# Kernel tuning notes

Measured on AMD Instinct MI355X. Metric: run time of the kernel, lower is better.

Reference implementation:

```python
import jax, jax.numpy as jnp
import numpy as np

D_MODEL = 256
N_HEADS = 8
D_K = 16
LN_EPS = 1e-5


def setup_inputs() -> dict:
    key = jax.random.key(0)
    ks = jax.random.split(key, 10)
    B, S = 4, 2048
    inp = {
        "input_Q": jax.random.normal(ks[0], (B, S, D_MODEL), dtype=jnp.float32),
        "input_K": jax.random.normal(ks[1], (B, S, D_MODEL), dtype=jnp.float32),
        "input_V": jax.random.normal(ks[2], (B, S, D_MODEL), dtype=jnp.float32),
        "attn_mask": jax.random.randint(ks[3], (B, S, S), 0, 2) == 1,
        # learned params (torch Linear weight [out,in] stored here as [in,out])
        "Wq": jax.random.normal(ks[4], (D_MODEL, N_HEADS * D_K), dtype=jnp.float32) * (1.0 / np.sqrt(D_MODEL)),
        "Wk": jax.random.normal(ks[5], (D_MODEL, N_HEADS * D_K), dtype=jnp.float32) * (1.0 / np.sqrt(D_MODEL)),
        "Wv": jax.random.normal(ks[6], (D_MODEL, N_HEADS * D_K), dtype=jnp.float32) * (1.0 / np.sqrt(D_MODEL)),
        "Wfc": jax.random.normal(ks[7], (N_HEADS * D_K, D_MODEL), dtype=jnp.float32) * (1.0 / np.sqrt(N_HEADS * D_K)),
        "ln_gamma": jnp.ones((D_MODEL,), dtype=jnp.float32),
        "ln_beta": jnp.zeros((D_MODEL,), dtype=jnp.float32),
    }
    return inp


def reference(input_Q, input_K, input_V, attn_mask, Wq, Wk, Wv, Wfc, ln_gamma, ln_beta):
    B, S, _ = input_Q.shape
    # projections -> [B, H, S, d_k]
    Q = (input_Q @ Wq).reshape(B, S, N_HEADS, D_K).transpose(0, 2, 1, 3)
    K = (input_K @ Wk).reshape(B, S, N_HEADS, D_K).transpose(0, 2, 1, 3)
    V = (input_V @ Wv).reshape(B, S, N_HEADS, D_K).transpose(0, 2, 1, 3)
    # scores [B, H, S, S], masked softmax
    scores = jnp.einsum("bhqd,bhkd->bhqk", Q, K) / np.sqrt(D_K).astype(np.float32)
    scores = jnp.where(attn_mask[:, None, :, :], jnp.float32(-1e9), scores)
    attn = jax.nn.softmax(scores, axis=-1)
    context = jnp.einsum("bhqk,bhkd->bhqd", attn, V)
    context = context.transpose(0, 2, 1, 3).reshape(B, S, N_HEADS * D_K)
    out = context @ Wfc
    # LayerNorm (no residual in the original module)
    mu = jnp.mean(out, axis=-1, keepdims=True)
    var = jnp.var(out, axis=-1, keepdims=True)
    out = (out - mu) * jax.lax.rsqrt(var + LN_EPS) * ln_gamma + ln_beta
    return out
```

## Files before the change

### kernel.cpp

```cpp
#include <hip/hip_runtime.h>
#include <hip/hip_bf16.h>

#define S_LEN 2048
#define BATCH 4
#define NH 8
#define DK 16
#define DM 256
#define DP 128
#define L2E 1.4426950408889634f
#define MAGIC_BOOL 0x600DB001

typedef short bf16x8 __attribute__((ext_vector_type(8)));
typedef short short4v __attribute__((ext_vector_type(4)));
typedef float f32x16 __attribute__((ext_vector_type(16)));

__device__ __forceinline__ short f2bf(float x) {
    __hip_bfloat16 h = __float2bfloat16(x);
    return __builtin_bit_cast(short, h);
}

union Frag { bf16x8 v; short4v h2[2]; };

__global__ __launch_bounds__(256) void setup(
    const unsigned int* __restrict__ mrawu, int* __restrict__ flag,
    const float* __restrict__ Wq, const float* __restrict__ Wk,
    const float* __restrict__ Wv, short* __restrict__ Wt)
{
    const int bi = blockIdx.x;
    if (bi < 1024) {
        unsigned int u = mrawu[bi * 256 + threadIdx.x];
        if (u & 0xFFFFFF00u) *flag = MAGIC_BOOL;
    } else {
        const int tid = (bi - 1024) * 256 + threadIdx.x;
        const int m = tid >> 15;
        const int rem = tid & 32767;
        const int k = rem >> 7, c = rem & 127;
        const float* W = (m == 0) ? Wq : (m == 1) ? Wk : Wv;
        const float scale = (m == 0) ? 0.25f * L2E : 1.0f;
        Wt[((size_t)m * 128 + c) * 256 + k] = f2bf(W[(size_t)k * 128 + c] * scale);
    }
}

__global__ __launch_bounds__(256) void phase1(
    const void* __restrict__ mraw, const int* __restrict__ flag,
    unsigned long long* __restrict__ ms64,
    const float* __restrict__ Xq, const float* __restrict__ Xk, const float* __restrict__ Xv,
    const short* __restrict__ Wt,
    short* __restrict__ Qb, short* __restrict__ Kb, short* __restrict__ Vb)
{
    __shared__ short xs_s[32 * 260];
    const int bi = blockIdx.x;
    const int t = threadIdx.x;

    if (bi < 768) {
        const int inp = bi >> 8;
        const int s0 = (bi & 255) * 32;
        {
            const float* xsrc = ((inp == 0) ? Xq : (inp == 1) ? Xk : Xv)
                              + (size_t)(s0 + (t >> 3)) * 256 + (t & 7) * 32;
            short* xdst = &xs_s[(t >> 3) * 260 + (t & 7) * 32];
            #pragma unroll
            for (int u = 0; u < 8; ++u) {
                float4 xv = *(const float4*)(xsrc + u * 4);
                short4v o = { f2bf(xv.x), f2bf(xv.y), f2bf(xv.z), f2bf(xv.w) };
                *(short4v*)(xdst + u * 4) = o;
            }
        }
        __syncthreads();

        const int wave = t >> 6, lane = t & 63;
        const int lq = lane & 31, hi = lane >> 5;
        const int c = wave * 32 + lq;
        const short* wrow = Wt + ((size_t)inp * 128 + c) * 256;

        f32x16 acc;
        #pragma unroll
        for (int i = 0; i < 16; ++i) acc[i] = 0.f;

        #pragma unroll
        for (int kb = 0; kb < 16; ++kb) {
            Frag af, bf_;
            af.h2[0]  = *(const short4v*)&xs_s[lq * 260 + kb*16 + 4*hi];
            af.h2[1]  = *(const short4v*)&xs_s[lq * 260 + kb*16 + 8 + 4*hi];
            bf_.h2[0] = *(const short4v*)(wrow + kb*16 + 4*hi);
            bf_.h2[1] = *(const short4v*)(wrow + kb*16 + 8 + 4*hi);
            acc = __builtin_amdgcn_mfma_f32_32x32x16_bf16(af.v, bf_.v, acc, 0, 0, 0);
        }

        const int b = s0 >> 11, sl = s0 & (S_LEN - 1);
        const int h = c >> 4, d = c & 15;
        if (inp < 2) {
            short* dst = (inp == 0) ? Qb : Kb;
            #pragma unroll
            for (int r = 0; r < 16; ++r) {
                const int s = sl + (r & 3) + 8*(r >> 2) + 4*hi;
                dst[(((size_t)(b * NH + h)) * S_LEN + s) * DK + d] = f2bf(acc[r]);
            }
        } else {
            short* vb = Vb + (((size_t)(b * NH + h)) * 32 + d) * S_LEN + sl;
            #pragma unroll
            for (int g = 0; g < 4; ++g) {
                short4v vv = { f2bf(acc[4*g]), f2bf(acc[4*g+1]), f2bf(acc[4*g+2]), f2bf(acc[4*g+3]) };
                *(short4v*)(vb + 8*g + 4*hi) = vv;
            }
        }
    } else if (bi < 1280) {
        const int tid = (bi - 768) * 256 + t;
        const int bh = tid >> 12;
        const int rem = tid & 4095;
        const int row = 16 + (rem >> 11) * 4;
        const int s = rem & 2047;
        Vb[((size_t)bh * 32 + row) * S_LEN + s] = (short)0x3F80;
    } else {
        const int lane = t & 63;
        const size_t kbase = ((size_t)(bi - 1280) * 4 + (t >> 6)) * 256;
        const int isInt = (*flag != MAGIC_BOOL);

        int v[4];
        if (isInt) {
            const int* p = (const int*)mraw + kbase + lane;
            #pragma unroll
            for (int g = 0; g < 4; ++g) v[g] = p[g * 64];
        } else {
            const unsigned char* p = (const unsigned char*)mraw + kbase + lane;
            #pragma unroll
            for (int g = 0; g < 4; ++g) v[g] = p[g * 64];
        }

        const int src = 32*((lane>>5)&1) + 4*((lane>>4)&1) + 8*((lane>>2)&3) + (lane&3);
        const size_t row = kbase >> 11;
        const int koff0 = (int)(kbase & 2047);

        #pragma unroll
        for (int g = 0; g < 4; ++g) {
            const unsigned long long W = __ballot(v[g] != 0);
            const unsigned long long W2 = __ballot((int)((W >> src) & 1ull));
            if (lane == 0) {
                const int koff = koff0 + g * 64;
                ms64[(size_t)(koff >> 7) * (BATCH*S_LEN*2) + row*2 + ((koff >> 6) & 1)] = W2;
            }
        }
    }
}

__global__ __launch_bounds__(256, 8) void attn_mfma(
    const short* __restrict__ Qb, const short* __restrict__ Kb, const short* __restrict__ Vb,
    const unsigned int* __restrict__ ms, float* __restrict__ pacc, float* __restrict__ pl)
{
    __shared__ short kt_s[128 * 20];
    __shared__ short vt_s[32 * 132];

    const int bh = blockIdx.y;
    const int b = bh >> 3;
    const int z = blockIdx.z;
    const int t = threadIdx.x;
    const int wave = t >> 6, lane = t & 63;
    const int lq = lane & 31, hi = lane >> 5;
    const int qrow = blockIdx.x * 128 + wave * 32 + lq;
    const int hish = hi * 16;

    Frag qf;
    {
        const short* qp = Qb + ((size_t)bh * S_LEN + qrow) * DK;
        qf.h2[0] = *(const short4v*)(qp + 4*hi);
        qf.h2[1] = *(const short4v*)(qp + 8 + 4*hi);
    }

    f32x16 acc;
    #pragma unroll
    for (int i = 0; i < 16; ++i) acc[i] = 0.f;

    const short* kbase = Kb + (size_t)bh * S_LEN * DK;
    const short* vbase = Vb + (size_t)bh * 32 * S_LEN;
    const unsigned int* mbase = ms + ((size_t)b * S_LEN + qrow) * 4;

    const int tiles = (S_LEN / 128) / gridDim.z;
    const int t0 = z * tiles, t1 = t0 + tiles;

    for (int tile = t0; tile < t1; ++tile) {
        const int k0 = tile * 128;

        {
            const uint4 kv = *(const uint4*)(kbase + (size_t)k0 * DK + t * 8);
            short* kdst = &kt_s[(t >> 1) * 20 + (t & 1) * 8];
            *(uint2*)(kdst)     = *(uint2*)&kv;
            *(uint2*)(kdst + 4) = *((uint2*)&kv + 1);

            const short* vsrc = vbase + (size_t)(t >> 3) * S_LEN + k0 + (t & 7) * 16;
            uint4 v0 = *(const uint4*)(vsrc);
            uint4 v1 = *(const uint4*)(vsrc + 8);
            short* vdst = &vt_s[(t >> 3) * 132 + (t & 7) * 16];
            *(uint2*)(vdst)      = *(uint2*)&v0;
            *(uint2*)(vdst + 4)  = *((uint2*)&v0 + 1);
            *(uint2*)(vdst + 8)  = *(uint2*)&v1;
            *(uint2*)(vdst + 12) = *((uint2*)&v1 + 1);
        }
        __syncthreads();

        const uint4 mw = *(const uint4*)(mbase + (size_t)tile * (BATCH * S_LEN * 4));

        #pragma unroll
        for (int kt = 0; kt < 4; ++kt) {
            const unsigned int W = ((kt==0)?mw.x:(kt==1)?mw.y:(kt==2)?mw.z:mw.w) >> hish;
            f32x16 ci;
            #pragma unroll
            for (int r = 0; r < 16; ++r)
                ci[r] = __int_as_float(((int)(W << (31 - r)) >> 31) & 0xC2C80000);

            Frag kf;
            kf.h2[0] = *(const short4v*)&kt_s[(kt*32 + lq) * 20 + 4*hi];
            kf.h2[1] = *(const short4v*)&kt_s[(kt*32 + lq) * 20 + 8 + 4*hi];
            f32x16 p = __builtin_amdgcn_mfma_f32_32x32x16_bf16(kf.v, qf.v, ci, 0, 0, 0);

            #pragma unroll
            for (int r = 0; r < 16; ++r) p[r] = __builtin_amdgcn_exp2f(p[r]);

            #pragma unroll
            for (int j = 0; j < 2; ++j) {
                union { bf16x8 v; short s[8]; } pf;
                #pragma unroll
                for (int e = 0; e < 8; ++e) pf.s[e] = f2bf(p[j*8 + e]);
                Frag vf;
                const int vo = lq * 132 + (kt*2 + j) * 16 + 4*hi;
                vf.h2[0] = *(const short4v*)&vt_s[vo];
                vf.h2[1] = *(const short4v*)&vt_s[vo + 8];
                acc = __builtin_amdgcn_mfma_f32_32x32x16_bf16(vf.v, pf.v, acc, 0, 0, 0);
            }
        }
        __syncthreads();
    }

    float* pb = pacc + (((size_t)z * (BATCH*NH) + bh) * S_LEN + qrow) * 16;
    float4 o1 = { acc[0], acc[1], acc[2], acc[3] };
    float4 o2 = { acc[4], acc[5], acc[6], acc[7] };
    *(float4*)(pb + 4*hi) = o1;
    *(float4*)(pb + 8 + 4*hi) = o2;
    if (hi == 0) pl[((size_t)z * (BATCH*NH) + bh) * S_LEN + qrow] = acc[8];
}

__global__ __launch_bounds__(256) void fc_ln(
    const float* __restrict__ pacc, const float* __restrict__ pl, int ns,
    const float* __restrict__ Wfc,
    const float* __restrict__ gamma, const float* __restrict__ beta,
    float* __restrict__ out)
{
    __shared__ float cs[8][DP];
    __shared__ float ys[8][256];
    __shared__ float red[16];
    const int t = threadIdx.x;
    const int row0 = blockIdx.x * 8;

    {
        const int idx = t * 4;
        const int r = idx >> 7, k = idx & 127;
        const int grow = row0 + r;
        const int b = grow >> 11, q = grow & (S_LEN - 1);
        const int h = k >> 4, d0 = k & 15;
        float4 s = {0.f, 0.f, 0.f, 0.f};
        float L = 0.f;
        for (int z = 0; z < ns; ++z) {
            const size_t o = ((size_t)z * (BATCH*NH) + b * NH + h) * S_LEN + q;
            const float4 a = *(const float4*)(pacc + o * 16 + d0);
            s.x += a.x; s.y += a.y; s.z += a.z; s.w += a.w;
            L += pl[o];
        }
        const float inv = 1.0f / L;
        float4 o4 = { s.x * inv, s.y * inv, s.z * inv, s.w * inv };
        *(float4*)&cs[r][k] = o4;
    }
    __syncthreads();

    float acc[8] = {0,0,0,0,0,0,0,0};
    for (int k = 0; k < DP; k += 4) {
        const float w0 = Wfc[(k+0)*DM + t];
        const float w1 = Wfc[(k+1)*DM + t];
        const float w2 = Wfc[(k+2)*DM + t];
        const float w3 = Wfc[(k+3)*DM + t];
        #pragma unroll
        for (int r = 0; r < 8; ++r) {
            float4 x = *(const float4*)&cs[r][k];
            acc[r] = fmaf(x.x, w0, fmaf(x.y, w1, fmaf(x.z, w2, fmaf(x.w, w3, acc[r]))));
        }
    }

    #pragma unroll
    for (int r = 0; r < 8; ++r) ys[r][t] = acc[r];
    __syncthreads();

    const int w = t >> 6, lj = t & 63;
    #pragma unroll
    for (int rr = 0; rr < 2; ++rr) {
        const int r = w * 2 + rr;
        float a0 = ys[r][lj], a1 = ys[r][lj+64], a2 = ys[r][lj+128], a3 = ys[r][lj+192];
        float s1 = a0 + a1 + a2 + a3;
        float s2 = a0*a0 + a1*a1 + a2*a2 + a3*a3;
        #pragma unroll
        for (int off = 32; off; off >>= 1) {
            s1 += __shfl_xor(s1, off);
            s2 += __shfl_xor(s2, off);
        }
        if (lj == 0) {
            float mu = s1 * (1.0f/256.0f);
            float var = s2 * (1.0f/256.0f) - mu*mu;
            red[r*2]     = mu;
            red[r*2 + 1] = rsqrtf(var + 1e-5f);
        }
    }
    __syncthreads();

    const float g = gamma[t], be = beta[t];
    #pragma unroll
    for (int r = 0; r < 8; ++r) {
        float y = (acc[r] - red[r*2]) * red[r*2 + 1];
        out[(size_t)(row0 + r) * DM + t] = fmaf(y, g, be);
    }
}

extern "C" void kernel_launch(void* const* d_in, const int* in_sizes, int n_in,
                              void* d_out, int out_size, void* d_ws, size_t ws_size,
                              hipStream_t stream)
{
    const float* Xq = (const float*)d_in[0];
    const float* Xk = (const float*)d_in[1];
    const float* Xv = (const float*)d_in[2];
    const void* mask_raw = d_in[3];
    const float* Wq  = (const float*)d_in[4];
    const float* Wk  = (const float*)d_in[5];
    const float* Wv  = (const float*)d_in[6];
    const float* Wfc = (const float*)d_in[7];
    const float* gamma = (const float*)d_in[8];
    const float* beta  = (const float*)d_in[9];
    float* out = (float*)d_out;

    const size_t headsz = (size_t)BATCH * NH * S_LEN * DK;
    const size_t maskelems = (size_t)BATCH * S_LEN * S_LEN;

    char* wsb = (char*)d_ws;
    short* Qb = (short*)wsb;
    short* Kb = Qb + headsz;
    short* Vb = Kb + headsz;
    unsigned short* msk = (unsigned short*)(Vb + 2 * headsz);
    short* Wt = (short*)(msk + maskelems / 16);
    float* pacc = (float*)(Wt + 3 * 128 * 256);
    size_t ns = 4;
    {
        const size_t fixed = (size_t)((char*)pacc - wsb);
        while (ns > 1 && fixed + ns * ((size_t)BATCH*NH*S_LEN*17*4) + 64 > ws_size)
            ns >>= 1;
    }
    float* pl = pacc + ns * (size_t)BATCH * NH * S_LEN * 16;
    int* flag = (int*)(pl + ns * (size_t)BATCH * NH * S_LEN);

    setup<<<dim3(1408), dim3(256), 0, stream>>>(
        (const unsigned int*)mask_raw, flag, Wq, Wk, Wv, Wt);
    phase1<<<dim3(768 + 512 + (unsigned)(maskelems / 1024)), dim3(256), 0, stream>>>(
        mask_raw, flag, (unsigned long long*)msk, Xq, Xk, Xv, Wt, Qb, Kb, Vb);
    attn_mfma<<<dim3(S_LEN / 128, BATCH * NH, (unsigned)ns), dim3(256), 0, stream>>>(
        Qb, Kb, Vb, (const unsigned int*)msk, pacc, pl);
    fc_ln<<<dim3(BATCH * S_LEN / 8), dim3(256), 0, stream>>>(pacc, pl, (int)ns, Wfc, gamma, beta, out);
}
```

Measured before the change: 85.71 us.

## Store Q transposed, drop mask bit-permute ballot, coarsen mask packing blocks

Q is now written in a transposed [bh][d][s] layout using vectorized short4 stores like V, and the attention kernel gathers it with strided scalar loads. The mask packer drops its second permuting ballot and stores raw ballot words. The attention kernel instead decodes the bit order per row from two 64-bit words. Each mask-packing wave now handles 1024 elements instead of 256, so fewer blocks are launched. The X staging loads are also reordered to be fully coalesced. The goal is to cut scattered global stores and ballot work in phase1, at the cost of uncoalesced Q loads that happen once per thread.

New measurement: 81.65 us. 4.7% less time.

```diff
diff --git a/kernel.cpp b/kernel.cpp
--- a/kernel.cpp
+++ b/kernel.cpp
@@ -46,7 +46,7 @@
     unsigned long long* __restrict__ ms64,
     const float* __restrict__ Xq, const float* __restrict__ Xk, const float* __restrict__ Xv,
     const short* __restrict__ Wt,
-    short* __restrict__ Qb, short* __restrict__ Kb, short* __restrict__ Vb)
+    short* __restrict__ Qt, short* __restrict__ Kb, short* __restrict__ Vb)
 {
     __shared__ short xs_s[32 * 260];
     const int bi = blockIdx.x;
@@ -56,14 +56,14 @@
         const int inp = bi >> 8;
         const int s0 = (bi & 255) * 32;
         {
-            const float* xsrc = ((inp == 0) ? Xq : (inp == 1) ? Xk : Xv)
-                              + (size_t)(s0 + (t >> 3)) * 256 + (t & 7) * 32;
-            short* xdst = &xs_s[(t >> 3) * 260 + (t & 7) * 32];
+            const float* xbase = ((inp == 0) ? Xq : (inp == 1) ? Xk : Xv) + (size_t)s0 * 256;
             #pragma unroll
             for (int u = 0; u < 8; ++u) {
-                float4 xv = *(const float4*)(xsrc + u * 4);
+                const int idx = u * 1024 + t * 4;
+                const int row = idx >> 8, col = idx & 255;
+                float4 xv = *(const float4*)(xbase + idx);
                 short4v o = { f2bf(xv.x), f2bf(xv.y), f2bf(xv.z), f2bf(xv.w) };
-                *(short4v*)(xdst + u * 4) = o;
+                *(short4v*)&xs_s[row * 260 + col] = o;
             }
         }
         __syncthreads();
@@ -89,19 +89,20 @@
 
         const int b = s0 >> 11, sl = s0 & (S_LEN - 1);
         const int h = c >> 4, d = c & 15;
-        if (inp < 2) {
-            short* dst = (inp == 0) ? Qb : Kb;
+        if (inp == 1) {
             #pragma unroll
             for (int r = 0; r < 16; ++r) {
                 const int s = sl + (r & 3) + 8*(r >> 2) + 4*hi;
-                dst[(((size_t)(b * NH + h)) * S_LEN + s) * DK + d] = f2bf(acc[r]);
+                Kb[(((size_t)(b * NH + h)) * S_LEN + s) * DK + d] = f2bf(acc[r]);
             }
         } else {
-            short* vb = Vb + (((size_t)(b * NH + h)) * 32 + d) * S_LEN + sl;
+            short* base = (inp == 0)
+                ? Qt + (((size_t)(b * NH + h)) * 16 + d) * S_LEN + sl
+                : Vb + (((size_t)(b * NH + h)) * 32 + d) * S_LEN + sl;
             #pragma unroll
             for (int g = 0; g < 4; ++g) {
                 short4v vv = { f2bf(acc[4*g]), f2bf(acc[4*g+1]), f2bf(acc[4*g+2]), f2bf(acc[4*g+3]) };
-                *(short4v*)(vb + 8*g + 4*hi) = vv;
+                *(short4v*)(base + 8*g + 4*hi) = vv;
             }
         }
     } else if (bi < 1280) {
@@ -113,39 +114,37 @@
         Vb[((size_t)bh * 32 + row) * S_LEN + s] = (short)0x3F80;
     } else {
         const int lane = t & 63;
-        const size_t kbase = ((size_t)(bi - 1280) * 4 + (t >> 6)) * 256;
+        const size_t kbase = ((size_t)(bi - 1280) * 4 + (t >> 6)) * 1024;
         const int isInt = (*flag != MAGIC_BOOL);
 
-        int v[4];
+        int v[16];
         if (isInt) {
             const int* p = (const int*)mraw + kbase + lane;
             #pragma unroll
-            for (int g = 0; g < 4; ++g) v[g] = p[g * 64];
+            for (int g = 0; g < 16; ++g) v[g] = p[g * 64];
         } else {
             const unsigned char* p = (const unsigned char*)mraw + kbase + lane;
             #pragma unroll
-            for (int g = 0; g < 4; ++g) v[g] = p[g * 64];
-        }
-
-        const int src = 32*((lane>>5)&1) + 4*((lane>>4)&1) + 8*((lane>>2)&3) + (lane&3);
+            for (int g = 0; g < 16; ++g) v[g] = p[g * 64];
+        }
+
         const size_t row = kbase >> 11;
         const int koff0 = (int)(kbase & 2047);
 
         #pragma unroll
-        for (int g = 0; g < 4; ++g) {
+        for (int g = 0; g < 16; ++g) {
             const unsigned long long W = __ballot(v[g] != 0);
-            const unsigned long long W2 = __ballot((int)((W >> src) & 1ull));
             if (lane == 0) {
                 const int koff = koff0 + g * 64;
-                ms64[(size_t)(koff >> 7) * (BATCH*S_LEN*2) + row*2 + ((koff >> 6) & 1)] = W2;
+                ms64[(size_t)(koff >> 7) * (BATCH*S_LEN*2) + row*2 + ((koff >> 6) & 1)] = W;
             }
         }
     }
 }
 
 __global__ __launch_bounds__(256, 8) void attn_mfma(
-    const short* __restrict__ Qb, const short* __restrict__ Kb, const short* __restrict__ Vb,
-    const unsigned int* __restrict__ ms, float* __restrict__ pacc, float* __restrict__ pl)
+    const short* __restrict__ Qt, const short* __restrict__ Kb, const short* __restrict__ Vb,
+    const unsigned long long* __restrict__ ms64, float* __restrict__ pacc, float* __restrict__ pl)
 {
     __shared__ short kt_s[128 * 20];
     __shared__ short vt_s[32 * 132];
@@ -157,13 +156,15 @@
     const int wave = t >> 6, lane = t & 63;
     const int lq = lane & 31, hi = lane >> 5;
     const int qrow = blockIdx.x * 128 + wave * 32 + lq;
-    const int hish = hi * 16;
 
     Frag qf;
     {
-        const short* qp = Qb + ((size_t)bh * S_LEN + qrow) * DK;
-        qf.h2[0] = *(const short4v*)(qp + 4*hi);
-        qf.h2[1] = *(const short4v*)(qp + 8 + 4*hi);
+        const short* qt = Qt + (size_t)bh * 16 * S_LEN + qrow;
+        #pragma unroll
+        for (int j = 0; j < 4; ++j) {
+            qf.h2[0][j] = qt[(size_t)(4*hi + j) * S_LEN];
+            qf.h2[1][j] = qt[(size_t)(8 + 4*hi + j) * S_LEN];
+        }
     }
 
     f32x16 acc;
@@ -172,7 +173,7 @@
 
     const short* kbase = Kb + (size_t)bh * S_LEN * DK;
     const short* vbase = Vb + (size_t)bh * 32 * S_LEN;
-    const unsigned int* mbase = ms + ((size_t)b * S_LEN + qrow) * 4;
+    const unsigned long long* mbase = ms64 + ((size_t)b * S_LEN + qrow) * 2;
 
     const int tiles = (S_LEN / 128) / gridDim.z;
     const int t0 = z * tiles, t1 = t0 + tiles;
@@ -197,15 +198,19 @@
         }
         __syncthreads();
 
-        const uint4 mw = *(const uint4*)(mbase + (size_t)tile * (BATCH * S_LEN * 4));
+        const unsigned long long* mw = mbase + (size_t)tile * (BATCH * S_LEN * 2);
+        const unsigned long long W64a = mw[0], W64b = mw[1];
 
         #pragma unroll
         for (int kt = 0; kt < 4; ++kt) {
-            const unsigned int W = ((kt==0)?mw.x:(kt==1)?mw.y:(kt==2)?mw.z:mw.w) >> hish;
+            const unsigned int W = (unsigned int)(((kt < 2) ? W64a : W64b)
+                                                  >> (32*(kt & 1) + 4*hi));
             f32x16 ci;
             #pragma unroll
-            for (int r = 0; r < 16; ++r)
-                ci[r] = __int_as_float(((int)(W << (31 - r)) >> 31) & 0xC2C80000);
+            for (int r = 0; r < 16; ++r) {
+                const int bit = (r & 3) + 8*(r >> 2);
+                ci[r] = __int_as_float(((int)(W << (31 - bit)) >> 31) & 0xC2C80000);
+            }
 
             Frag kf;
             kf.h2[0] = *(const short4v*)&kt_s[(kt*32 + lq) * 20 + 4*hi];
@@ -336,11 +341,11 @@
     const size_t maskelems = (size_t)BATCH * S_LEN * S_LEN;
 
     char* wsb = (char*)d_ws;
-    short* Qb = (short*)wsb;
-    short* Kb = Qb + headsz;
+    short* Qt = (short*)wsb;
+    short* Kb = Qt + headsz;
     short* Vb = Kb + headsz;
-    unsigned short* msk = (unsigned short*)(Vb + 2 * headsz);
-    short* Wt = (short*)(msk + maskelems / 16);
+    unsigned long long* msk = (unsigned long long*)(Vb + 2 * headsz);
+    short* Wt = (short*)(msk + maskelems / 64);
     float* pacc = (float*)(Wt + 3 * 128 * 256);
     size_t ns = 4;
     {
@@ -353,9 +358,9 @@
 
     setup<<<dim3(1408), dim3(256), 0, stream>>>(
         (const unsigned int*)mask_raw, flag, Wq, Wk, Wv, Wt);
-    phase1<<<dim3(768 + 512 + (unsigned)(maskelems / 1024)), dim3(256), 0, stream>>>(
-        mask_raw, flag, (unsigned long long*)msk, Xq, Xk, Xv, Wt, Qb, Kb, Vb);
+    phase1<<<dim3(768 + 512 + (unsigned)(maskelems / 4096)), dim3(256), 0, stream>>>(
+        mask_raw, flag, msk, Xq, Xk, Xv, Wt, Qt, Kb, Vb);
     attn_mfma<<<dim3(S_LEN / 128, BATCH * NH, (unsigned)ns), dim3(256), 0, stream>>>(
-        Qb, Kb, Vb, (const unsigned int*)msk, pacc, pl);
+        Qt, Kb, Vb, msk, pacc, pl);
     fc_ln<<<dim3(BATCH * S_LEN / 8), dim3(256), 0, stream>>>(pacc, pl, (int)ns, Wfc, gamma, beta, out);
 }
```
